# Kernel optimization log

Hardware: AMD Instinct MI355X
Metric: run time of the kernel (lower is better)

## Reference

```python
import jax, jax.numpy as jnp
import numpy as np

C = 512
HSIZE = C // 4
D, H, W = 18, 24, 24
N = D * H * W


def setup_inputs() -> dict:
    key = jax.random.key(0)
    ks = jax.random.split(key, 6)
    features = jax.random.normal(ks[0], (1, C, D, H, W), dtype=jnp.float32)
    Wi = jax.random.normal(ks[1], (HSIZE, C), dtype=jnp.float32) * 0.02
    bi = jax.random.normal(ks[2], (HSIZE,), dtype=jnp.float32) * 0.02
    Wj = jax.random.normal(ks[3], (HSIZE, C), dtype=jnp.float32) * 0.02
    bj = jax.random.normal(ks[4], (HSIZE,), dtype=jnp.float32) * 0.02
    # attention_agregate: shape (head=1, 1), xavier-uniform in the original
    agg = jax.random.uniform(ks[5], (1, 1), dtype=jnp.float32, minval=-1.0, maxval=1.0)
    return {"features": features, "Wi": Wi, "bi": bi, "Wj": Wj, "bj": bj, "agg": agg}


def reference(features, Wi, bi, Wj, bj, agg):
    # features: [1, C, D, H, W]; 1x1x1 convs == channel-wise matmuls
    x = features.reshape(C, N)                      # [C, N]
    fi = (Wi @ x + bi[:, None]).T                   # [N, hsize]  (conv_i output, permuted)
    fj = Wj @ x + bj[:, None]                       # [hsize, N]  (conv_j output)
    fk = x.T                                        # [N, C]      (raw features, NOT conv_k)
    # original: attn = (fi @ fj) * agg / N ; out = attn @ fk
    # linear chain reassociated: fi @ (fj @ fk) * agg / N  (same math, no NxN intermediate)
    scale = agg[0, 0] / jnp.float32(N)
    out_flat = (fi @ (fj @ fk)) * scale             # [N, C]
    return features + out_flat.T.reshape(1, C, D, H, W)
```

## Files before the change

kernel.cpp:

```cpp
#include <hip/hip_runtime.h>
#include <hip/hip_bf16.h>

#define C_   512
#define HS   128
#define NN   10368

typedef __bf16 bf16x8 __attribute__((ext_vector_type(8)));
typedef __bf16 bf16x2 __attribute__((ext_vector_type(2)));
typedef float  f32x4  __attribute__((ext_vector_type(4)));

__device__ __forceinline__ bf16x8 load_f32x8_as_bf16(const float* __restrict__ p) {
    float4 v0 = *(const float4*)p;
    float4 v1 = *(const float4*)(p + 4);
    bf16x8 o;
    o[0] = (__bf16)v0.x; o[1] = (__bf16)v0.y; o[2] = (__bf16)v0.z; o[3] = (__bf16)v0.w;
    o[4] = (__bf16)v1.x; o[5] = (__bf16)v1.y; o[6] = (__bf16)v1.z; o[7] = (__bf16)v1.w;
    return o;
}

__global__ __launch_bounds__(256, 2)
void k_fused12(const float* __restrict__ feat,
               const float* __restrict__ Wi, const float* __restrict__ Wj,
               const float* __restrict__ bi, const float* __restrict__ bj,
               __bf16* __restrict__ xb, __bf16* __restrict__ fj,
               __bf16* __restrict__ finm, float* __restrict__ Mtf) {
    const int b = blockIdx.x;
    const int t = threadIdx.x;
    if (b >= 324) {
        const int j = b - 324;
        f32x4 z = {0.f, 0.f, 0.f, 0.f};
        float* p = Mtf + j * 4096 + t * 16;
        *(f32x4*)(p) = z; *(f32x4*)(p + 4) = z;
        *(f32x4*)(p + 8) = z; *(f32x4*)(p + 12) = z;
        return;
    }
    __shared__ __bf16 xt[32][520];
    const int n0 = b * 32;
    {
        const int tn = t & 31;
        const int c2 = (t >> 5) * 2;
        #pragma unroll
        for (int half = 0; half < 2; half++) {
            float va[16], vb[16];
            const int base = half * 256;
            #pragma unroll
            for (int p = 0; p < 16; p++) {
                const int c = base + p * 16 + c2;
                va[p] = feat[(size_t)c * NN + n0 + tn];
                vb[p] = feat[(size_t)(c + 1) * NN + n0 + tn];
            }
            #pragma unroll
            for (int p = 0; p < 16; p++) {
                const int c = base + p * 16 + c2;
                __bf16 b0 = (__bf16)va[p], b1 = (__bf16)vb[p];
                xb[(size_t)c * NN + n0 + tn]       = b0;
                xb[(size_t)(c + 1) * NN + n0 + tn] = b1;
                bf16x2 pk; pk[0] = b0; pk[1] = b1;
                *(bf16x2*)&xt[tn][c] = pk;
            }
        }
    }
    __syncthreads();
    const int w    = t >> 6;
    const int lane = t & 63;
    const int l16  = lane & 15;
    const int q    = lane >> 4;
    const int h0   = w * 32;
    f32x4 afj[2][2] = {};
    f32x4 afi[2][2] = {};
    #pragma unroll 4
    for (int k = 0; k < 512; k += 32) {
        bf16x8 ln[2], wj[2], wi[2];
        #pragma unroll
        for (int i = 0; i < 2; i++)
            ln[i] = *(const bf16x8*)&xt[16 * i + l16][k + q * 8];
        #pragma unroll
        for (int i = 0; i < 2; i++)
            wj[i] = load_f32x8_as_bf16(Wj + (h0 + 16 * i + l16) * 512 + k + q * 8);
        #pragma unroll
        for (int i = 0; i < 2; i++)
            wi[i] = load_f32x8_as_bf16(Wi + (h0 + 16 * i + l16) * 512 + k + q * 8);
        #pragma unroll
        for (int i = 0; i < 2; i++)
            #pragma unroll
            for (int tt = 0; tt < 2; tt++) {
                afj[i][tt] = __builtin_amdgcn_mfma_f32_16x16x32_bf16(wj[i], ln[tt], afj[i][tt], 0, 0, 0);
                afi[i][tt] = __builtin_amdgcn_mfma_f32_16x16x32_bf16(ln[i], wi[tt], afi[i][tt], 0, 0, 0);
            }
    }
    float4 bjv[2];
    bjv[0] = *(const float4*)(bj + h0 + q * 4);
    bjv[1] = *(const float4*)(bj + h0 + 16 + q * 4);
    float biv[2];
    biv[0] = bi[h0 + l16];
    biv[1] = bi[h0 + 16 + l16];
    #pragma unroll
    for (int i = 0; i < 2; i++)
        #pragma unroll
        for (int tt = 0; tt < 2; tt++)
            #pragma unroll
            for (int r = 0; r < 4; r++) {
                {
                    int h = h0 + 16 * i + q * 4 + r;
                    int n = n0 + 16 * tt + l16;
                    fj[(size_t)h * NN + n] = (__bf16)(afj[i][tt][r] + (&bjv[i].x)[r]);
                }
                {
                    int n = n0 + 16 * i + q * 4 + r;
                    int h = h0 + 16 * tt + l16;
                    finm[(size_t)n * HS + h] = (__bf16)(afi[i][tt][r] + biv[tt]);
                }
            }
}

__global__ __launch_bounds__(256, 2)
void k_gemm3(const __bf16* __restrict__ xb, const __bf16* __restrict__ fj,
             float* __restrict__ Mtf) {
    __shared__ float red[4][64][17];
    const int b    = blockIdx.x;
    const int t    = threadIdx.x;
    const int v    = t >> 6;
    const int lane = t & 63;
    const int l16  = lane & 15;
    const int q    = lane >> 4;
    const int tile = b & 63, g = b >> 6;
    const int c0 = (tile >> 2) * 32, h0 = (tile & 3) * 32;
    const int chunk = g * 4 + v;
    const int s0 = (chunk * 324) >> 5;
    const int s1 = ((chunk + 1) * 324) >> 5;
    f32x4 acc[2][2] = {};
    bf16x8 a[2], bb[2];
    {
        const int k = s0 * 32;
        a[0]  = *(const bf16x8*)(xb + (size_t)(c0 + l16) * NN + k + q * 8);
        a[1]  = *(const bf16x8*)(xb + (size_t)(c0 + 16 + l16) * NN + k + q * 8);
        bb[0] = *(const bf16x8*)(fj + (size_t)(h0 + l16) * NN + k + q * 8);
        bb[1] = *(const bf16x8*)(fj + (size_t)(h0 + 16 + l16) * NN + k + q * 8);
    }
    for (int s = s0; s < s1 - 1; s++) {
        const int kn = (s + 1) * 32;
        bf16x8 a2[2], b2[2];
        a2[0] = *(const bf16x8*)(xb + (size_t)(c0 + l16) * NN + kn + q * 8);
        a2[1] = *(const bf16x8*)(xb + (size_t)(c0 + 16 + l16) * NN + kn + q * 8);
        b2[0] = *(const bf16x8*)(fj + (size_t)(h0 + l16) * NN + kn + q * 8);
        b2[1] = *(const bf16x8*)(fj + (size_t)(h0 + 16 + l16) * NN + kn + q * 8);
        #pragma unroll
        for (int i = 0; i < 2; i++)
            #pragma unroll
            for (int tt = 0; tt < 2; tt++)
                acc[i][tt] = __builtin_amdgcn_mfma_f32_16x16x32_bf16(a[i], bb[tt], acc[i][tt], 0, 0, 0);
        a[0] = a2[0]; a[1] = a2[1]; bb[0] = b2[0]; bb[1] = b2[1];
    }
    #pragma unroll
    for (int i = 0; i < 2; i++)
        #pragma unroll
        for (int tt = 0; tt < 2; tt++)
            acc[i][tt] = __builtin_amdgcn_mfma_f32_16x16x32_bf16(a[i], bb[tt], acc[i][tt], 0, 0, 0);
    #pragma unroll
    for (int i = 0; i < 2; i++)
        #pragma unroll
        for (int tt = 0; tt < 2; tt++)
            #pragma unroll
            for (int r = 0; r < 4; r++)
                red[v][lane][i * 8 + tt * 4 + r] = acc[i][tt][r];
    __syncthreads();
    #pragma unroll
    for (int u = 0; u < 4; u++) {
        const int idx = t * 4 + u;
        const int lane_e = idx >> 4, j = idx & 15;
        float s = red[0][lane_e][j] + red[1][lane_e][j]
                + red[2][lane_e][j] + red[3][lane_e][j];
        const int i = j >> 3, tt = (j >> 2) & 1, r = j & 3;
        const int qe = lane_e >> 4, le = lane_e & 15;
        const int c = c0 + 16 * i + qe * 4 + r;
        const int h = h0 + 16 * tt + le;
        atomicAdd(&Mtf[c * HS + h], s);
    }
}

__global__ __launch_bounds__(256, 2)
void k_gemm4(const float* __restrict__ Mtf, const __bf16* __restrict__ finm,
             const float* __restrict__ feat, const float* __restrict__ agg,
             float* __restrict__ out) {
    const int w    = blockIdx.x * 4 + (threadIdx.x >> 6);
    const int lane = threadIdx.x & 63;
    const int l16  = lane & 15;
    const int q    = lane >> 4;
    const int c0 = (w & 15) * 32, n0 = (w >> 4) * 64;
    const float scale = agg[0] * (1.0f / (float)NN);
    f32x4 acc[2][4] = {};
    #pragma unroll
    for (int k = 0; k < 128; k += 32) {
        bf16x8 a[2], b[4];
        #pragma unroll
        for (int i = 0; i < 2; i++)
            a[i] = load_f32x8_as_bf16(Mtf + (c0 + 16 * i + l16) * HS + k + q * 8);
        #pragma unroll
        for (int tt = 0; tt < 4; tt++)
            b[tt] = *(const bf16x8*)(finm + (size_t)(n0 + 16 * tt + l16) * HS + k + q * 8);
        #pragma unroll
        for (int i = 0; i < 2; i++)
            #pragma unroll
            for (int tt = 0; tt < 4; tt++)
                acc[i][tt] = __builtin_amdgcn_mfma_f32_16x16x32_bf16(a[i], b[tt], acc[i][tt], 0, 0, 0);
    }
    float fv[2][4][4];
    #pragma unroll
    for (int i = 0; i < 2; i++)
        #pragma unroll
        for (int tt = 0; tt < 4; tt++)
            #pragma unroll
            for (int r = 0; r < 4; r++) {
                const int c = c0 + 16 * i + q * 4 + r;
                const int n = n0 + 16 * tt + l16;
                fv[i][tt][r] = feat[(size_t)c * NN + n];
            }
    #pragma unroll
    for (int i = 0; i < 2; i++)
        #pragma unroll
        for (int tt = 0; tt < 4; tt++)
            #pragma unroll
            for (int r = 0; r < 4; r++) {
                const int c = c0 + 16 * i + q * 4 + r;
                const int n = n0 + 16 * tt + l16;
                out[(size_t)c * NN + n] = fv[i][tt][r] + scale * acc[i][tt][r];
            }
}

extern "C" void kernel_launch(void* const* d_in, const int* in_sizes, int n_in,
                              void* d_out, int out_size, void* d_ws, size_t ws_size,
                              hipStream_t stream) {
    const float* feat = (const float*)d_in[0];
    const float* Wi   = (const float*)d_in[1];
    const float* bi   = (const float*)d_in[2];
    const float* Wj   = (const float*)d_in[3];
    const float* bj   = (const float*)d_in[4];
    const float* agg  = (const float*)d_in[5];
    float* out = (float*)d_out;

    char* ws = (char*)d_ws;
    __bf16* xb   = (__bf16*)(ws);
    __bf16* fj   = (__bf16*)(ws + 10616832);
    __bf16* finm = (__bf16*)(ws + 13271040);
    float*  Mtf  = (float*) (ws + 15925248);

    k_fused12<<<340, 256, 0, stream>>>(feat, Wi, Wj, bi, bj, xb, fj, finm, Mtf);
    k_gemm3 <<<512, 256, 0, stream>>>(xb, fj, Mtf);
    k_gemm4 <<<648, 256, 0, stream>>>(Mtf, finm, feat, agg, out);
}
```

Baseline: 139.7 us.

## Precast weights to bf16, vectorize feature loads, stage gemm4 epilogue through LDS

```diff
diff --git a/kernel.cpp b/kernel.cpp
--- a/kernel.cpp
+++ b/kernel.cpp
@@ -6,6 +6,7 @@
 #define NN   10368
 
 typedef __bf16 bf16x8 __attribute__((ext_vector_type(8)));
+typedef __bf16 bf16x4 __attribute__((ext_vector_type(4)));
 typedef __bf16 bf16x2 __attribute__((ext_vector_type(2)));
 typedef float  f32x4  __attribute__((ext_vector_type(4)));
 
@@ -19,45 +20,59 @@
 }
 
 __global__ __launch_bounds__(256, 2)
+void k_prep(const float* __restrict__ Wi, const float* __restrict__ Wj,
+            __bf16* __restrict__ Wib, __bf16* __restrict__ Wjb,
+            float* __restrict__ Mtf) {
+    const int b = blockIdx.x;
+    const int t = threadIdx.x;
+    if (b < 4) {
+        const float* src = (b < 2) ? Wj : Wi;
+        __bf16* dst = (b < 2) ? Wjb : Wib;
+        const int off = (b & 1) * 32768;
+        #pragma unroll 4
+        for (int u = 0; u < 32; u++) {
+            const int idx = off + u * 1024 + t * 4;
+            float4 v = *(const float4*)(src + idx);
+            bf16x4 o;
+            o[0] = (__bf16)v.x; o[1] = (__bf16)v.y;
+            o[2] = (__bf16)v.z; o[3] = (__bf16)v.w;
+            *(bf16x4*)(dst + idx) = o;
+        }
+    } else {
+        const int z = b - 4;
+        f32x4 zv = {0.f, 0.f, 0.f, 0.f};
+        float* p = Mtf + z * 4096 + t * 16;
+        *(f32x4*)(p) = zv; *(f32x4*)(p + 4) = zv;
+        *(f32x4*)(p + 8) = zv; *(f32x4*)(p + 12) = zv;
+    }
+}
+
+__global__ __launch_bounds__(256, 2)
 void k_fused12(const float* __restrict__ feat,
-               const float* __restrict__ Wi, const float* __restrict__ Wj,
+               const __bf16* __restrict__ Wib, const __bf16* __restrict__ Wjb,
                const float* __restrict__ bi, const float* __restrict__ bj,
                __bf16* __restrict__ xb, __bf16* __restrict__ fj,
-               __bf16* __restrict__ finm, float* __restrict__ Mtf) {
+               __bf16* __restrict__ finm) {
     const int b = blockIdx.x;
     const int t = threadIdx.x;
-    if (b >= 324) {
-        const int j = b - 324;
-        f32x4 z = {0.f, 0.f, 0.f, 0.f};
-        float* p = Mtf + j * 4096 + t * 16;
-        *(f32x4*)(p) = z; *(f32x4*)(p + 4) = z;
-        *(f32x4*)(p + 8) = z; *(f32x4*)(p + 12) = z;
-        return;
-    }
     __shared__ __bf16 xt[32][520];
     const int n0 = b * 32;
     {
-        const int tn = t & 31;
-        const int c2 = (t >> 5) * 2;
-        #pragma unroll
-        for (int half = 0; half < 2; half++) {
-            float va[16], vb[16];
-            const int base = half * 256;
-            #pragma unroll
-            for (int p = 0; p < 16; p++) {
-                const int c = base + p * 16 + c2;
-                va[p] = feat[(size_t)c * NN + n0 + tn];
-                vb[p] = feat[(size_t)(c + 1) * NN + n0 + tn];
-            }
-            #pragma unroll
-            for (int p = 0; p < 16; p++) {
-                const int c = base + p * 16 + c2;
-                __bf16 b0 = (__bf16)va[p], b1 = (__bf16)vb[p];
-                xb[(size_t)c * NN + n0 + tn]       = b0;
-                xb[(size_t)(c + 1) * NN + n0 + tn] = b1;
-                bf16x2 pk; pk[0] = b0; pk[1] = b1;
-                *(bf16x2*)&xt[tn][c] = pk;
-            }
+        const int g  = t & 7;
+        const int c8 = t >> 3;
+        const int nq = 4 * g;
+        #pragma unroll
+        for (int p = 0; p < 16; p++) {
+            const int c = c8 + 32 * p;
+            float4 v = *(const float4*)(feat + (size_t)c * NN + n0 + nq);
+            bf16x4 o;
+            o[0] = (__bf16)v.x; o[1] = (__bf16)v.y;
+            o[2] = (__bf16)v.z; o[3] = (__bf16)v.w;
+            *(bf16x4*)(xb + (size_t)c * NN + n0 + nq) = o;
+            xt[nq + 0][c] = o[0];
+            xt[nq + 1][c] = o[1];
+            xt[nq + 2][c] = o[2];
+            xt[nq + 3][c] = o[3];
         }
     }
     __syncthreads();
@@ -76,10 +91,10 @@
             ln[i] = *(const bf16x8*)&xt[16 * i + l16][k + q * 8];
         #pragma unroll
         for (int i = 0; i < 2; i++)
-            wj[i] = load_f32x8_as_bf16(Wj + (h0 + 16 * i + l16) * 512 + k + q * 8);
-        #pragma unroll
-        for (int i = 0; i < 2; i++)
-            wi[i] = load_f32x8_as_bf16(Wi + (h0 + 16 * i + l16) * 512 + k + q * 8);
+            wj[i] = *(const bf16x8*)&Wjb[(size_t)(h0 + 16 * i + l16) * C_ + k + q * 8];
+        #pragma unroll
+        for (int i = 0; i < 2; i++)
+            wi[i] = *(const bf16x8*)&Wib[(size_t)(h0 + 16 * i + l16) * C_ + k + q * 8];
         #pragma unroll
         for (int i = 0; i < 2; i++)
             #pragma unroll
@@ -182,8 +197,11 @@
 void k_gemm4(const float* __restrict__ Mtf, const __bf16* __restrict__ finm,
              const float* __restrict__ feat, const float* __restrict__ agg,
              float* __restrict__ out) {
-    const int w    = blockIdx.x * 4 + (threadIdx.x >> 6);
-    const int lane = threadIdx.x & 63;
+    __shared__ float lds_out[128][64];
+    const int t    = threadIdx.x;
+    const int wv   = t >> 6;
+    const int w    = blockIdx.x * 4 + wv;
+    const int lane = t & 63;
     const int l16  = lane & 15;
     const int q    = lane >> 4;
     const int c0 = (w & 15) * 32, n0 = (w >> 4) * 64;
@@ -191,40 +209,49 @@
     f32x4 acc[2][4] = {};
     #pragma unroll
     for (int k = 0; k < 128; k += 32) {
-        bf16x8 a[2], b[4];
+        bf16x8 a[2], bfr[4];
         #pragma unroll
         for (int i = 0; i < 2; i++)
             a[i] = load_f32x8_as_bf16(Mtf + (c0 + 16 * i + l16) * HS + k + q * 8);
         #pragma unroll
         for (int tt = 0; tt < 4; tt++)
-            b[tt] = *(const bf16x8*)(finm + (size_t)(n0 + 16 * tt + l16) * HS + k + q * 8);
+            bfr[tt] = *(const bf16x8*)(finm + (size_t)(n0 + 16 * tt + l16) * HS + k + q * 8);
         #pragma unroll
         for (int i = 0; i < 2; i++)
             #pragma unroll
             for (int tt = 0; tt < 4; tt++)
-                acc[i][tt] = __builtin_amdgcn_mfma_f32_16x16x32_bf16(a[i], b[tt], acc[i][tt], 0, 0, 0);
-    }
-    float fv[2][4][4];
+                acc[i][tt] = __builtin_amdgcn_mfma_f32_16x16x32_bf16(a[i], bfr[tt], acc[i][tt], 0, 0, 0);
+    }
     #pragma unroll
     for (int i = 0; i < 2; i++)
         #pragma unroll
         for (int tt = 0; tt < 4; tt++)
             #pragma unroll
-            for (int r = 0; r < 4; r++) {
-                const int c = c0 + 16 * i + q * 4 + r;
-                const int n = n0 + 16 * tt + l16;
-                fv[i][tt][r] = feat[(size_t)c * NN + n];
-            }
-    #pragma unroll
-    for (int i = 0; i < 2; i++)
-        #pragma unroll
-        for (int tt = 0; tt < 4; tt++)
-            #pragma unroll
-            for (int r = 0; r < 4; r++) {
-                const int c = c0 + 16 * i + q * 4 + r;
-                const int n = n0 + 16 * tt + l16;
-                out[(size_t)c * NN + n] = fv[i][tt][r] + scale * acc[i][tt][r];
-            }
+            for (int r = 0; r < 4; r++)
+                lds_out[wv * 32 + 16 * i + q * 4 + r][16 * tt + l16] = scale * acc[i][tt][r];
+    __syncthreads();
+    const int c0b = ((blockIdx.x * 4) & 15) * 32;
+    const int n0b = ((blockIdx.x * 4) >> 4) * 64;
+    #pragma unroll
+    for (int rr = 0; rr < 2; rr++) {
+        const int row = (t >> 2) + 64 * rr;
+        const size_t gbase = (size_t)(c0b + row) * NN + n0b;
+        float4 fv[4];
+        #pragma unroll
+        for (int j4 = 0; j4 < 4; j4++) {
+            const int col = (t & 3) * 4 + j4 * 16;
+            fv[j4] = *(const float4*)(feat + gbase + col);
+        }
+        #pragma unroll
+        for (int j4 = 0; j4 < 4; j4++) {
+            const int col = (t & 3) * 4 + j4 * 16;
+            f32x4 v = *(const f32x4*)&lds_out[row][col];
+            float4 o;
+            o.x = fv[j4].x + v[0]; o.y = fv[j4].y + v[1];
+            o.z = fv[j4].z + v[2]; o.w = fv[j4].w + v[3];
+            *(float4*)(out + gbase + col) = o;
+        }
+    }
 }
 
 extern "C" void kernel_launch(void* const* d_in, const int* in_sizes, int n_in,
@@ -243,8 +270,11 @@
     __bf16* fj   = (__bf16*)(ws + 10616832);
     __bf16* finm = (__bf16*)(ws + 13271040);
     float*  Mtf  = (float*) (ws + 15925248);
-
-    k_fused12<<<340, 256, 0, stream>>>(feat, Wi, Wj, bi, bj, xb, fj, finm, Mtf);
-    k_gemm3 <<<512, 256, 0, stream>>>(xb, fj, Mtf);
-    k_gemm4 <<<648, 256, 0, stream>>>(Mtf, finm, feat, agg, out);
-}
+    __bf16* Wjb  = (__bf16*)(ws + 16187392);
+    __bf16* Wib  = (__bf16*)(ws + 16318464);
+
+    k_prep   <<<20,  256, 0, stream>>>(Wi, Wj, Wib, Wjb, Mtf);
+    k_fused12<<<324, 256, 0, stream>>>(feat, Wib, Wjb, bi, bj, xb, fj, finm);
+    k_gemm3  <<<512, 256, 0, stream>>>(xb, fj, Mtf);
+    k_gemm4  <<<648, 256, 0, stream>>>(Mtf, finm, feat, agg, out);
+}
```

New measurement: 129.2 us. 1.08x faster.
